# Kernel optimization log

Hardware: AMD Instinct MI355X
Metric: run time of the kernel (lower is better)

## Reference

```python
import jax, jax.numpy as jnp
import numpy as np

N_HEADS = 8

def setup_inputs() -> dict:
    key = jax.random.key(0)
    ks = jax.random.split(key, 8)
    N, D, H = 20000, 16, 256
    scale = np.float32(0.02)
    return {
        "h": jax.random.normal(ks[0], (N, H), dtype=jnp.float32),
        "attention_mask": jnp.zeros((N,), dtype=jnp.float32),
        "neighbor_idx": jax.random.randint(ks[1], (N, D), 0, N, dtype=jnp.int32),
        "Wq": jax.random.normal(ks[2], (H, H), dtype=jnp.float32) * scale,
        "bq": jnp.zeros((H,), dtype=jnp.float32),
        "Wk": jax.random.normal(ks[3], (H, H), dtype=jnp.float32) * scale,
        "bk": jnp.zeros((H,), dtype=jnp.float32),
        "Wv": jax.random.normal(ks[4], (H, H), dtype=jnp.float32) * scale,
        "bv": jnp.zeros((H,), dtype=jnp.float32),
    }

def reference(h, attention_mask, neighbor_idx, Wq, bq, Wk, bk, Wv, bv):
    N, H = h.shape
    nh = N_HEADS
    dh = H // nh
    inv_sqrt_dh = np.float32(1.0 / np.sqrt(dh))
    # query from each node's own state: [N, nh, dh]
    q = (h @ Wq.T + bq).reshape(N, nh, dh)
    # gather neighbor mailbox: [N, D, H]
    nb = h[neighbor_idx]
    k = (nb @ Wk.T + bk).reshape(N, -1, nh, dh)  # [N, D, nh, dh]
    v = (nb @ Wv.T + bv).reshape(N, -1, nh, dh)
    # scores: [N, nh, D]
    scores = jnp.einsum('nhd,nkhd->nhk', q, k) * inv_sqrt_dh
    # additive mask gathered from source nodes, broadcast over heads
    scores = scores + attention_mask[neighbor_idx][:, None, :]
    probs = jax.nn.softmax(scores, axis=-1)
    # dropout prob = 0.0 (eval) -> identity
    ctx = jnp.einsum('nhk,nkhd->nhd', probs, v).reshape(N, H)
    return ctx
```

## Files before the change

kernel.cpp:

```cpp
#include <hip/hip_runtime.h>
#include <math.h>

#define HDIM 256
#define DNEIGH 16

typedef __attribute__((ext_vector_type(8))) short short8;
typedef __attribute__((ext_vector_type(4))) float f32x4;

static __device__ __forceinline__ unsigned short f2bf(float f) {
    unsigned int u = __float_as_uint(f);
    unsigned int r = (u + 0x7fffu + ((u >> 16) & 1u)) >> 16;
    return (unsigned short)r;
}
static __device__ __forceinline__ float bf_lo(unsigned int u) {
    return __uint_as_float(u << 16);
}
static __device__ __forceinline__ float bf_hi(unsigned int u) {
    return __uint_as_float(u & 0xffff0000u);
}

static __device__ __forceinline__ void async_copy16(const void* g, void* l) {
    __builtin_amdgcn_global_load_lds(
        (const __attribute__((address_space(1))) unsigned int*)g,
        (__attribute__((address_space(3))) unsigned int*)l, 16, 0, 0);
}

__global__ __launch_bounds__(256) void cvt_kernel(
    const float* __restrict__ h,
    const float* __restrict__ wq, const float* __restrict__ wk, const float* __restrict__ wv,
    unsigned short* __restrict__ hb,
    unsigned short* __restrict__ wqb, unsigned short* __restrict__ wkb, unsigned short* __restrict__ wvb,
    int nh4)
{
    const int stride = gridDim.x * blockDim.x;
    const int total = nh4 + 3 * 16384;
    for (int i = blockIdx.x * blockDim.x + threadIdx.x; i < total; i += stride) {
        const float4* src; unsigned short* dst; int off;
        if (i < nh4) { src = (const float4*)h; dst = hb; off = i; }
        else {
            int j = i - nh4; int s = j >> 14; off = j & 16383;
            src = (s == 0) ? (const float4*)wq : (s == 1) ? (const float4*)wk : (const float4*)wv;
            dst = (s == 0) ? wqb : (s == 1) ? wkb : wvb;
        }
        float4 v = src[off];
        ushort4 o;
        o.x = f2bf(v.x); o.y = f2bf(v.y); o.z = f2bf(v.z); o.w = f2bf(v.w);
        *(ushort4*)&dst[off * 4] = o;
    }
}

__global__ __launch_bounds__(256) void qkv_mfma_kernel(
    const unsigned short* __restrict__ hb,
    const unsigned short* __restrict__ Wqb,
    const unsigned short* __restrict__ Wkb,
    const unsigned short* __restrict__ Wvb,
    const float* __restrict__ bq, const float* __restrict__ bk, const float* __restrict__ bv,
    float* __restrict__ Q, unsigned short* __restrict__ Kb, unsigned short* __restrict__ Vb,
    int N)
{
    __shared__ unsigned short As[128 * 64];
    __shared__ unsigned short Bs[128 * 64];

    const int t = threadIdx.x;
    const int lane = t & 63;
    const int wid = t >> 6;
    const int wm = wid >> 1;
    const int wn = wid & 1;
    const int m0 = blockIdx.x * 128;
    const int o0 = blockIdx.y * 128;
    const int sel = o0 >> 8;
    const int wrow0 = o0 & 255;

    const unsigned short* __restrict__ W = (sel == 0) ? Wqb : (sel == 1) ? Wkb : Wvb;
    const float* __restrict__ bias = (sel == 0) ? bq : (sel == 1) ? bk : bv;

    const int srow = lane >> 3;
    const int cg = (lane & 7) ^ srow;

    f32x4 acc[4][4] = {};

    for (int k0 = 0; k0 < HDIM; k0 += 64) {
#pragma unroll
        for (int r = 0; r < 4; ++r) {
            int rowb = wid * 32 + r * 8;
            const unsigned short* gp = &hb[(size_t)(m0 + rowb + srow) * HDIM + k0 + cg * 8];
            async_copy16(gp, &As[rowb * 64]);
        }
#pragma unroll
        for (int r = 0; r < 4; ++r) {
            int rowb = wid * 32 + r * 8;
            const unsigned short* gp = &W[(size_t)(wrow0 + rowb + srow) * HDIM + k0 + cg * 8];
            async_copy16(gp, &Bs[rowb * 64]);
        }
        __syncthreads();

#pragma unroll
        for (int ks = 0; ks < 2; ++ks) {
            short8 af[4], bf[4];
#pragma unroll
            for (int i = 0; i < 4; ++i) {
                int m = wm * 64 + i * 16 + (lane & 15);
                int chunk = (ks * 4 + (lane >> 4)) ^ (m & 7);
                af[i] = *(const short8*)&As[m * 64 + chunk * 8];
            }
#pragma unroll
            for (int j = 0; j < 4; ++j) {
                int n = wn * 64 + j * 16 + (lane & 15);
                int chunk = (ks * 4 + (lane >> 4)) ^ (n & 7);
                bf[j] = *(const short8*)&Bs[n * 64 + chunk * 8];
            }
#pragma unroll
            for (int i = 0; i < 4; ++i)
#pragma unroll
                for (int j = 0; j < 4; ++j)
                    acc[i][j] = __builtin_amdgcn_mfma_f32_16x16x32_bf16(af[i], bf[j], acc[i][j], 0, 0, 0);
        }
        __syncthreads();
    }

#pragma unroll
    for (int i = 0; i < 4; ++i) {
        int mbase = m0 + wm * 64 + i * 16 + (lane >> 4) * 4;
#pragma unroll
        for (int j = 0; j < 4; ++j) {
            int col = wrow0 + wn * 64 + j * 16 + (lane & 15);
            float b = bias[col];
#pragma unroll
            for (int r = 0; r < 4; ++r) {
                int gr = mbase + r;
                if (gr < N) {
                    float v = acc[i][j][r] + b;
                    if (sel == 0)       Q[(size_t)gr * HDIM + col] = v;
                    else if (sel == 1)  Kb[(size_t)gr * HDIM + col] = f2bf(v);
                    else                Vb[(size_t)gr * HDIM + col] = f2bf(v);
                }
            }
        }
    }
}

__global__ __launch_bounds__(256) void attn2_kernel(
    const float* __restrict__ Q,
    const unsigned short* __restrict__ Kb,
    const unsigned short* __restrict__ Vb,
    const float* __restrict__ mask,
    const int* __restrict__ nidx,
    float* __restrict__ out,
    int N)
{
    const int w = threadIdx.x >> 6;
    const int lane = threadIdx.x & 63;
    const int n = blockIdx.x * 4 + w;
    if (n >= N) return;

    int idl = nidx[(size_t)n * DNEIGH + (lane & 15)];
    float mskl = mask[idl];
    float4 q = *(const float4*)&Q[(size_t)n * HDIM + lane * 4];

    uint2 kreg[DNEIGH], vreg[DNEIGH];
#pragma unroll
    for (int d = 0; d < DNEIGH; ++d) {
        int id = __builtin_amdgcn_readlane(idl, d);
        kreg[d] = *(const uint2*)&Kb[(size_t)id * HDIM + lane * 4];
        vreg[d] = *(const uint2*)&Vb[(size_t)id * HDIM + lane * 4];
    }

    float e[DNEIGH];
    float s = 0.f;
#pragma unroll
    for (int d = 0; d < DNEIGH; ++d) {
        float p = q.x * bf_lo(kreg[d].x) + q.y * bf_hi(kreg[d].x)
                + q.z * bf_lo(kreg[d].y) + q.w * bf_hi(kreg[d].y);
        p += __shfl_xor(p, 1);
        p += __shfl_xor(p, 2);
        p += __shfl_xor(p, 4);
        float mk = __builtin_amdgcn_readlane(__float_as_int(mskl), d);
        mk = __int_as_float(__float_as_int(mk));
        float scr = p * 0.17677669529663688f + __int_as_float(__builtin_amdgcn_readlane(__float_as_int(mskl), d));
        e[d] = __expf(scr);
        s += e[d];
    }
    float rs = 1.f / s;

    float4 acc = make_float4(0.f, 0.f, 0.f, 0.f);
#pragma unroll
    for (int d = 0; d < DNEIGH; ++d) {
        float wgt = e[d] * rs;
        acc.x += wgt * bf_lo(vreg[d].x);
        acc.y += wgt * bf_hi(vreg[d].x);
        acc.z += wgt * bf_lo(vreg[d].y);
        acc.w += wgt * bf_hi(vreg[d].y);
    }
    *(float4*)&out[(size_t)n * HDIM + lane * 4] = acc;
}

extern "C" void kernel_launch(void* const* d_in, const int* in_sizes, int n_in,
                              void* d_out, int out_size, void* d_ws, size_t ws_size,
                              hipStream_t stream)
{
    const float* h    = (const float*)d_in[0];
    const float* mask = (const float*)d_in[1];
    const int*   nidx = (const int*)d_in[2];
    const float* Wq   = (const float*)d_in[3];
    const float* bq   = (const float*)d_in[4];
    const float* Wk   = (const float*)d_in[5];
    const float* bk   = (const float*)d_in[6];
    const float* Wv   = (const float*)d_in[7];
    const float* bv   = (const float*)d_in[8];

    const int N = in_sizes[0] / HDIM;

    char* ws = (char*)d_ws;
    float*          Qp  = (float*)ws;          ws += (size_t)N * HDIM * 4;
    unsigned short* Kbp = (unsigned short*)ws; ws += (size_t)N * HDIM * 2;
    unsigned short* Vbp = (unsigned short*)ws; ws += (size_t)N * HDIM * 2;
    unsigned short* hbp = (unsigned short*)ws; ws += (size_t)N * HDIM * 2;
    unsigned short* Wqb = (unsigned short*)ws; ws += 65536 * 2;
    unsigned short* Wkb = (unsigned short*)ws; ws += 65536 * 2;
    unsigned short* Wvb = (unsigned short*)ws;

    const int nh4 = (N * HDIM) / 4;
    cvt_kernel<<<1280, 256, 0, stream>>>(h, Wq, Wk, Wv, hbp, Wqb, Wkb, Wvb, nh4);

    dim3 g1((N + 127) / 128, 6);
    qkv_mfma_kernel<<<g1, 256, 0, stream>>>(hbp, Wqb, Wkb, Wvb, bq, bk, bv, Qp, Kbp, Vbp, N);

    attn2_kernel<<<(N + 3) / 4, 256, 0, stream>>>(Qp, Kbp, Vbp, mask, nidx, (float*)d_out, N);
}
```

Before: 160.3 us.

## Interleave K and V rows into one buffer for single 16-byte gathers

K and V projections are now written into one interleaved [N,512] bf16 buffer, so each neighbor row is fetched with a single 16-byte load per lane instead of two 8-byte loads. In the attention kernel, lanes 0-31 hold K and compute scores with 8-wide dot products and a shorter shuffle reduction. Lanes 32-63 hold V and receive the softmax weights through a cross-lane shuffle. This halves the number of gather instructions and improves contiguity per neighbor, at the cost of an extra shuffle per neighbor and half the lanes idling on the output store.

```diff
diff --git a/kernel.cpp b/kernel.cpp
--- a/kernel.cpp
+++ b/kernel.cpp
@@ -55,7 +55,7 @@
     const unsigned short* __restrict__ Wkb,
     const unsigned short* __restrict__ Wvb,
     const float* __restrict__ bq, const float* __restrict__ bk, const float* __restrict__ bv,
-    float* __restrict__ Q, unsigned short* __restrict__ Kb, unsigned short* __restrict__ Vb,
+    float* __restrict__ Q, unsigned short* __restrict__ KV,
     int N)
 {
     __shared__ unsigned short As[128 * 64];
@@ -131,18 +131,17 @@
                 if (gr < N) {
                     float v = acc[i][j][r] + b;
                     if (sel == 0)       Q[(size_t)gr * HDIM + col] = v;
-                    else if (sel == 1)  Kb[(size_t)gr * HDIM + col] = f2bf(v);
-                    else                Vb[(size_t)gr * HDIM + col] = f2bf(v);
+                    else if (sel == 1)  KV[(size_t)gr * 512 + col] = f2bf(v);
+                    else                KV[(size_t)gr * 512 + 256 + col] = f2bf(v);
                 }
             }
         }
     }
 }
 
-__global__ __launch_bounds__(256) void attn2_kernel(
+__global__ __launch_bounds__(256) void attn3_kernel(
     const float* __restrict__ Q,
-    const unsigned short* __restrict__ Kb,
-    const unsigned short* __restrict__ Vb,
+    const unsigned short* __restrict__ KV,
     const float* __restrict__ mask,
     const int* __restrict__ nidx,
     float* __restrict__ out,
@@ -155,43 +154,53 @@
 
     int idl = nidx[(size_t)n * DNEIGH + (lane & 15)];
     float mskl = mask[idl];
-    float4 q = *(const float4*)&Q[(size_t)n * HDIM + lane * 4];
-
-    uint2 kreg[DNEIGH], vreg[DNEIGH];
+
+    uint4 reg[DNEIGH];
 #pragma unroll
     for (int d = 0; d < DNEIGH; ++d) {
         int id = __builtin_amdgcn_readlane(idl, d);
-        kreg[d] = *(const uint2*)&Kb[(size_t)id * HDIM + lane * 4];
-        vreg[d] = *(const uint2*)&Vb[(size_t)id * HDIM + lane * 4];
-    }
+        reg[d] = *(const uint4*)&KV[(size_t)id * 512 + lane * 8];
+    }
+
+    int cq = (lane & 31) * 8;
+    float4 qa = *(const float4*)&Q[(size_t)n * HDIM + cq];
+    float4 qb = *(const float4*)&Q[(size_t)n * HDIM + cq + 4];
 
     float e[DNEIGH];
     float s = 0.f;
 #pragma unroll
     for (int d = 0; d < DNEIGH; ++d) {
-        float p = q.x * bf_lo(kreg[d].x) + q.y * bf_hi(kreg[d].x)
-                + q.z * bf_lo(kreg[d].y) + q.w * bf_hi(kreg[d].y);
+        float p = qa.x * bf_lo(reg[d].x) + qa.y * bf_hi(reg[d].x)
+                + qa.z * bf_lo(reg[d].y) + qa.w * bf_hi(reg[d].y)
+                + qb.x * bf_lo(reg[d].z) + qb.y * bf_hi(reg[d].z)
+                + qb.z * bf_lo(reg[d].w) + qb.w * bf_hi(reg[d].w);
         p += __shfl_xor(p, 1);
         p += __shfl_xor(p, 2);
-        p += __shfl_xor(p, 4);
-        float mk = __builtin_amdgcn_readlane(__float_as_int(mskl), d);
-        mk = __int_as_float(__float_as_int(mk));
-        float scr = p * 0.17677669529663688f + __int_as_float(__builtin_amdgcn_readlane(__float_as_int(mskl), d));
-        e[d] = __expf(scr);
+        float mk = __int_as_float(__builtin_amdgcn_readlane(__float_as_int(mskl), d));
+        e[d] = __expf(p * 0.17677669529663688f + mk);
         s += e[d];
     }
     float rs = 1.f / s;
 
-    float4 acc = make_float4(0.f, 0.f, 0.f, 0.f);
+    int src = (lane < 32) ? lane : (((lane - 32) >> 2) << 2);
+    float acc[8] = {0.f, 0.f, 0.f, 0.f, 0.f, 0.f, 0.f, 0.f};
 #pragma unroll
     for (int d = 0; d < DNEIGH; ++d) {
-        float wgt = e[d] * rs;
-        acc.x += wgt * bf_lo(vreg[d].x);
-        acc.y += wgt * bf_hi(vreg[d].x);
-        acc.z += wgt * bf_lo(vreg[d].y);
-        acc.w += wgt * bf_hi(vreg[d].y);
-    }
-    *(float4*)&out[(size_t)n * HDIM + lane * 4] = acc;
+        float wgt = __shfl(e[d] * rs, src);
+        acc[0] += wgt * bf_lo(reg[d].x);
+        acc[1] += wgt * bf_hi(reg[d].x);
+        acc[2] += wgt * bf_lo(reg[d].y);
+        acc[3] += wgt * bf_hi(reg[d].y);
+        acc[4] += wgt * bf_lo(reg[d].z);
+        acc[5] += wgt * bf_hi(reg[d].z);
+        acc[6] += wgt * bf_lo(reg[d].w);
+        acc[7] += wgt * bf_hi(reg[d].w);
+    }
+    if (lane >= 32) {
+        int co = (lane - 32) * 8;
+        *(float4*)&out[(size_t)n * HDIM + co]     = make_float4(acc[0], acc[1], acc[2], acc[3]);
+        *(float4*)&out[(size_t)n * HDIM + co + 4] = make_float4(acc[4], acc[5], acc[6], acc[7]);
+    }
 }
 
 extern "C" void kernel_launch(void* const* d_in, const int* in_sizes, int n_in,
@@ -212,8 +221,7 @@
 
     char* ws = (char*)d_ws;
     float*          Qp  = (float*)ws;          ws += (size_t)N * HDIM * 4;
-    unsigned short* Kbp = (unsigned short*)ws; ws += (size_t)N * HDIM * 2;
-    unsigned short* Vbp = (unsigned short*)ws; ws += (size_t)N * HDIM * 2;
+    unsigned short* KVp = (unsigned short*)ws; ws += (size_t)N * 512 * 2;
     unsigned short* hbp = (unsigned short*)ws; ws += (size_t)N * HDIM * 2;
     unsigned short* Wqb = (unsigned short*)ws; ws += 65536 * 2;
     unsigned short* Wkb = (unsigned short*)ws; ws += 65536 * 2;
@@ -223,7 +231,7 @@
     cvt_kernel<<<1280, 256, 0, stream>>>(h, Wq, Wk, Wv, hbp, Wqb, Wkb, Wvb, nh4);
 
     dim3 g1((N + 127) / 128, 6);
-    qkv_mfma_kernel<<<g1, 256, 0, stream>>>(hbp, Wqb, Wkb, Wvb, bq, bk, bv, Qp, Kbp, Vbp, N);
-
-    attn2_kernel<<<(N + 3) / 4, 256, 0, stream>>>(Qp, Kbp, Vbp, mask, nidx, (float*)d_out, N);
-}
+    qkv_mfma_kernel<<<g1, 256, 0, stream>>>(hbp, Wqb, Wkb, Wvb, bq, bk, bv, Qp, KVp, N);
+
+    attn3_kernel<<<(N + 3) / 4, 256, 0, stream>>>(Qp, KVp, mask, nidx, (float*)d_out, N);
+}
```

Result: no change. 160.2 us (-0.1%).
